# Optimization experiments

Hardware: AMD Instinct MI355X
Metric: run time of the kernel (lower is better)

## Reference

```python
import jax, jax.numpy as jnp
import numpy as np

N, E, F_IN, H, K = 100000, 1600000, 256, 128, 5


def setup_inputs() -> dict:
    key = jax.random.key(0)
    ks = jax.random.split(key, 24)

    def rn(k, shape, scale=0.05):
        return jax.random.normal(k, shape, dtype=jnp.float32) * scale

    inp = {
        "x": rn(ks[0], (N, F_IN), 1.0),
        "edge_index": jax.random.randint(ks[1], (2, E), 0, N, dtype=jnp.int64),
        "edge_attr": jax.random.uniform(ks[2], (N, K), dtype=jnp.float32),
        "pre_W": rn(ks[3], (F_IN, H)),
        "pre_b": jnp.zeros((H,), jnp.float32),
        "c1_Ws": rn(ks[4], (H, H)),
        "c1_Wn": rn(ks[5], (H, H)),
        "c1_b": jnp.zeros((H,), jnp.float32),
        "c2_Ws": rn(ks[6], (H, H)),
        "c2_Wn": rn(ks[7], (H, H)),
        "c2_b": jnp.zeros((H,), jnp.float32),
        "nodepost_W": rn(ks[8], (H, H)),
        "nodepost_b": jnp.zeros((H,), jnp.float32),
        "d_W0": rn(ks[9], (K, H)),
        "d_b0": jnp.zeros((H,), jnp.float32),
        "d_W1": rn(ks[10], (H, H)),
        "d_b1": jnp.zeros((H,), jnp.float32),
        "d_W2": rn(ks[11], (H, H)),
        "d_b2": jnp.zeros((H,), jnp.float32),
        "d_W3": rn(ks[12], (H, H)),
        "d_b3": jnp.zeros((H,), jnp.float32),
        "final_W": rn(ks[13], (2 * H, 1)),
        "final_b": jnp.zeros((1,), jnp.float32),
    }
    return inp


def _mean_agg(h, src, dst, n):
    # scatter-mean of source features onto destination nodes
    s = jax.ops.segment_sum(h[src], dst, num_segments=n)  # [N, H]
    deg = jax.ops.segment_sum(jnp.ones_like(dst, dtype=h.dtype), dst, num_segments=n)
    return s / jnp.maximum(deg, 1.0)[:, None]


def reference(x, edge_index, edge_attr, pre_W, pre_b,
              c1_Ws, c1_Wn, c1_b, c2_Ws, c2_Wn, c2_b,
              nodepost_W, nodepost_b,
              d_W0, d_b0, d_W1, d_b1, d_W2, d_b2, d_W3, d_b3,
              final_W, final_b):
    n = x.shape[0]
    src, dst = edge_index[0], edge_index[1]

    # --- feat path: NodeAttributeAggregator ---
    h = x @ pre_W + pre_b                                   # pre_process_mlp
    agg = _mean_agg(h, src, dst, n)
    h = jax.nn.relu(h @ c1_Ws + agg @ c1_Wn + c1_b)          # layer1 conv + act
    agg = _mean_agg(h, src, dst, n)
    h = jax.nn.relu(h @ c2_Ws + agg @ c2_Wn + c2_b)          # layer2 conv + act
    feat_out = h @ nodepost_W + nodepost_b                   # post_process_mlp

    # --- dist path: EdgeAttributeAggregator (MLP over edge attrs) ---
    e = edge_attr.reshape(-1, K)
    y = jax.nn.relu(e @ d_W0 + d_b0)
    y = jax.nn.relu(y @ d_W1 + d_b1)
    y = jax.nn.relu(y @ d_W2 + d_b2)
    dist_out = y @ d_W3 + d_b3

    # --- merge 'cat' + final MLP + squeeze + sigmoid ---
    z = jnp.concatenate([feat_out, dist_out], axis=1)        # [N, 2H]
    out = (z @ final_W + final_b).squeeze(1)                  # [N]
    return jax.nn.sigmoid(out)
```

## Files before the change

kernel.cpp:

```cpp
#include <hip/hip_runtime.h>

#define HF 128
#define CAP 64
#define PSHIFT 17
#define BUCKET_BLOCKS 2048

typedef __attribute__((ext_vector_type(8))) short s16x8;
typedef __attribute__((ext_vector_type(4))) float f32x4;
typedef __attribute__((ext_vector_type(2))) float f32x2;

__device__ __forceinline__ unsigned short f2bf(float f) {
    unsigned u = __float_as_uint(f);
    return (unsigned short)((u + 0x7fff + ((u >> 16) & 1)) >> 16);
}

#if __has_builtin(__builtin_amdgcn_cvt_pk_fp8_f32) && __has_builtin(__builtin_amdgcn_cvt_pk_f32_fp8)
#define FP8_HW 1
#else
#define FP8_HW 0
#endif

__device__ __forceinline__ unsigned char f2fp8(float f) {
#if FP8_HW
    int v = __builtin_amdgcn_cvt_pk_fp8_f32(f, f, 0, false);
    return (unsigned char)(v & 0xff);
#else
    unsigned u = __float_as_uint(f);
    unsigned s = (u >> 24) & 0x80;
    float a = fabsf(f);
    if (a > 448.f) a = 448.f;
    if (a < 0.015625f) {
        int q = (int)(a * 512.f + 0.5f);
        return (unsigned char)(s | q);
    }
    unsigned ub = __float_as_uint(a);
    ub += 0x0007ffff + ((ub >> 20) & 1);
    int e8 = (int)(ub >> 23) - 127 + 7;
    if (e8 >= 16) return (unsigned char)(s | 0x7e);
    return (unsigned char)(s | (e8 << 3) | ((ub >> 20) & 7));
#endif
}

__device__ __forceinline__ void fp8acc4(unsigned w, float* acc) {
#if FP8_HW
    f32x2 lo = __builtin_amdgcn_cvt_pk_f32_fp8(w, false);
    f32x2 hi = __builtin_amdgcn_cvt_pk_f32_fp8(w, true);
    acc[0] += lo.x; acc[1] += lo.y; acc[2] += hi.x; acc[3] += hi.y;
#else
    #pragma unroll
    for (int j = 0; j < 4; ++j) {
        unsigned b = (w >> (8 * j)) & 0xff;
        unsigned s = (b >> 7) & 1, e = (b >> 3) & 15, m = b & 7;
        float v = e ? __uint_as_float(((e + 120) << 23) | (m << 20))
                    : (float)m * 0.001953125f;
        acc[j] += s ? -v : v;
    }
#endif
}

__device__ __forceinline__ void repack_one(
    const float* __restrict__ W, short* __restrict__ Wp, int K, int t)
{
    int nkt = K >> 5;
    int lane = t & 63;
    int kt = (t >> 6) % nkt;
    int nt = (t >> 6) / nkt;
    int c = nt * 16 + (lane & 15);
    int kbase = kt * 32 + (lane >> 4) * 8;
    s16x8 v;
    #pragma unroll
    for (int j = 0; j < 8; ++j) v[j] = (short)f2bf(W[(long)(kbase + j) * HF + c]);
    *(s16x8*)(Wp + (long)t * 8) = v;
}

__global__ __launch_bounds__(256) void repack_all(
    const float* __restrict__ preW, const float* __restrict__ c1Ws,
    const float* __restrict__ c1Wn, const float* __restrict__ c2Ws,
    const float* __restrict__ c2Wn, const float* __restrict__ dW1,
    const float* __restrict__ dW2,
    short* preWp, short* c1Wsp, short* c1Wnp, short* c2Wsp, short* c2Wnp,
    short* dW1p, short* dW2p,
    const float* __restrict__ npW, const float* __restrict__ npb,
    const float* __restrict__ dW3, const float* __restrict__ db3,
    const float* __restrict__ fW,  const float* __restrict__ fb,
    float* __restrict__ uvc)
{
    int b = blockIdx.x;
    if (b == 64) {
        int i = threadIdx.x;
        if (i < HF) {
            float u = 0.f, v = 0.f;
            for (int j = 0; j < HF; ++j) {
                u += npW[i * HF + j] * fW[j];
                v += dW3[i * HF + j] * fW[HF + j];
            }
            uvc[i] = u;
            uvc[HF + i] = v;
            if (i == 0) {
                float c = fb[0];
                for (int j = 0; j < HF; ++j) c += npb[j] * fW[j] + db3[j] * fW[HF + j];
                uvc[2 * HF] = c;
            }
        }
        return;
    }
    if (b < 16) { repack_one(preW, preWp, 256, b * 256 + threadIdx.x); return; }
    int m = (b - 16) >> 3, t = ((b - 16) & 7) * 256 + threadIdx.x;
    const float* W; short* Wp;
    switch (m) {
        case 0: W = c1Ws; Wp = c1Wsp; break;
        case 1: W = c1Wn; Wp = c1Wnp; break;
        case 2: W = c2Ws; Wp = c2Wsp; break;
        case 3: W = c2Wn; Wp = c2Wnp; break;
        case 4: W = dW1;  Wp = dW1p;  break;
        default: W = dW2; Wp = dW2p;  break;
    }
    repack_one(W, Wp, HF, t);
}

__global__ __launch_bounds__(256) void bucketx_kernel(
    const int* __restrict__ eidx, long E,
    int* __restrict__ deg, int* __restrict__ bucket, int npass)
{
    const int xcd   = blockIdx.x & 7;
    const int chunk = blockIdx.x >> 3;
    const int nchunks = BUCKET_BLOCKS / 8;
    long per = (E + nchunks - 1) / nchunks;
    per = (per + 3) & ~3L;
    const long e0 = (long)chunk * per;
    const long e1 = (e0 + per < E) ? e0 + per : E;
    if (e0 >= E) return;
    for (int p = 0; p < npass; ++p) {
        for (long e = e0 + (long)threadIdx.x * 4; e + 4 <= e1; e += 1024) {
            int4 d4 = *(const int4*)(eidx + E + e);
            #pragma unroll
            for (int j = 0; j < 4; ++j) {
                int d = (&d4.x)[j];
                if ((d >> PSHIFT) != p || ((d >> 4) & 7) != xcd) continue;
                int s = eidx[e + j];
                int pos = atomicAdd(&deg[d], 1);
                if (pos < CAP) bucket[(long)d * CAP + pos] = s;
            }
        }
        for (long e = (e1 & ~3L) + threadIdx.x; e < e1; e += 256) {
            int d = eidx[E + e];
            if ((d >> PSHIFT) != p || ((d >> 4) & 7) != xcd) continue;
            int s = eidx[e];
            int pos = atomicAdd(&deg[d], 1);
            if (pos < CAP) bucket[(long)d * CAP + pos] = s;
        }
    }
}

__device__ __forceinline__ void agg_tile512(
    const unsigned char* __restrict__ hq, const int* __restrict__ deg,
    const int* __restrict__ bucket, int n, long row0B, int wv, int lane,
    unsigned* lds)
{
    const int g = lane >> 4;
    const int i = lane & 15;
    #pragma unroll
    for (int it = 0; it < 2; ++it) {
        const int rl = wv * 8 + it * 4 + g;
        const long node = row0B + rl;
        float acc[8];
        #pragma unroll
        for (int j = 0; j < 8; ++j) acc[j] = 0.f;
        int dg = 0, m = 0;
        const int* bl = bucket;
        if (node < n) {
            dg = deg[node];
            m = dg < CAP ? dg : CAP;
            bl = bucket + node * CAP;
        }
        int e = 0;
        for (; e + 8 <= m; e += 8) {
            int4 sa = *(const int4*)(bl + e);
            int4 sb = *(const int4*)(bl + e + 4);
            uint2 v0 = *(const uint2*)(hq + (long)sa.x * HF + i * 8);
            uint2 v1 = *(const uint2*)(hq + (long)sa.y * HF + i * 8);
            uint2 v2 = *(const uint2*)(hq + (long)sa.z * HF + i * 8);
            uint2 v3 = *(const uint2*)(hq + (long)sa.w * HF + i * 8);
            uint2 v4 = *(const uint2*)(hq + (long)sb.x * HF + i * 8);
            uint2 v5 = *(const uint2*)(hq + (long)sb.y * HF + i * 8);
            uint2 v6 = *(const uint2*)(hq + (long)sb.z * HF + i * 8);
            uint2 v7 = *(const uint2*)(hq + (long)sb.w * HF + i * 8);
            fp8acc4(v0.x, acc); fp8acc4(v0.y, acc + 4);
            fp8acc4(v1.x, acc); fp8acc4(v1.y, acc + 4);
            fp8acc4(v2.x, acc); fp8acc4(v2.y, acc + 4);
            fp8acc4(v3.x, acc); fp8acc4(v3.y, acc + 4);
            fp8acc4(v4.x, acc); fp8acc4(v4.y, acc + 4);
            fp8acc4(v5.x, acc); fp8acc4(v5.y, acc + 4);
            fp8acc4(v6.x, acc); fp8acc4(v6.y, acc + 4);
            fp8acc4(v7.x, acc); fp8acc4(v7.y, acc + 4);
        }
        for (; e + 4 <= m; e += 4) {
            int4 sa = *(const int4*)(bl + e);
            uint2 v0 = *(const uint2*)(hq + (long)sa.x * HF + i * 8);
            uint2 v1 = *(const uint2*)(hq + (long)sa.y * HF + i * 8);
            uint2 v2 = *(const uint2*)(hq + (long)sa.z * HF + i * 8);
            uint2 v3 = *(const uint2*)(hq + (long)sa.w * HF + i * 8);
            fp8acc4(v0.x, acc); fp8acc4(v0.y, acc + 4);
            fp8acc4(v1.x, acc); fp8acc4(v1.y, acc + 4);
            fp8acc4(v2.x, acc); fp8acc4(v2.y, acc + 4);
            fp8acc4(v3.x, acc); fp8acc4(v3.y, acc + 4);
        }
        for (; e < m; ++e) {
            uint2 v = *(const uint2*)(hq + (long)bl[e] * HF + i * 8);
            fp8acc4(v.x, acc); fp8acc4(v.y, acc + 4);
        }
        const float sc = 1.f / (float)(dg > 1 ? dg : 1);
        uint4 o;
        o.x = (unsigned)f2bf(acc[0] * sc) | ((unsigned)f2bf(acc[1] * sc) << 16);
        o.y = (unsigned)f2bf(acc[2] * sc) | ((unsigned)f2bf(acc[3] * sc) << 16);
        o.z = (unsigned)f2bf(acc[4] * sc) | ((unsigned)f2bf(acc[5] * sc) << 16);
        o.w = (unsigned)f2bf(acc[6] * sc) | ((unsigned)f2bf(acc[7] * sc) << 16);
        *(uint4*)&lds[rl * 64 + ((i ^ (rl & 15)) << 2)] = o;
    }
}

__device__ __forceinline__ void gemm_pass4(
    const unsigned short* __restrict__ Av, const short* __restrict__ Wp,
    long rA, int lane, int nb, f32x4 acc[4])
{
    const int q = lane >> 4;
    #pragma unroll
    for (int kt = 0; kt < 4; ++kt) {
        s16x8 a = *(const s16x8*)(Av + rA * HF + kt * 32 + q * 8);
        #pragma unroll
        for (int j = 0; j < 4; ++j) {
            s16x8 b = *(const s16x8*)(Wp + ((long)((nb + j) * 4 + kt) * 64 + lane) * 8);
            acc[j] = __builtin_amdgcn_mfma_f32_16x16x32_bf16(a, b, acc[j], 0, 0, 0);
        }
    }
}

__device__ __forceinline__ void gemm_pass_lds4(
    const unsigned* lds, int w3, int lane, const short* __restrict__ Wp,
    int nb, f32x4 acc[4])
{
    const int q = lane >> 4;
    const int i15 = lane & 15;
    const int rl = w3 * 16 + i15;
    #pragma unroll
    for (int kt = 0; kt < 4; ++kt) {
        s16x8 a = *(const s16x8*)&lds[rl * 64 + (((kt * 4 + q) ^ i15) << 2)];
        #pragma unroll
        for (int j = 0; j < 4; ++j) {
            s16x8 b = *(const s16x8*)(Wp + ((long)((nb + j) * 4 + kt) * 64 + lane) * 8);
            acc[j] = __builtin_amdgcn_mfma_f32_16x16x32_bf16(a, b, acc[j], 0, 0, 0);
        }
    }
}

__device__ __forceinline__ void gemm_pass_mfma8(
    const unsigned short* __restrict__ Av, const short* __restrict__ Wp,
    long rA, int lane, f32x4 acc[8])
{
    const int q = lane >> 4;
    #pragma unroll
    for (int kt = 0; kt < 4; ++kt) {
        s16x8 a = *(const s16x8*)(Av + rA * HF + kt * 32 + q * 8);
        #pragma unroll
        for (int nt = 0; nt < 8; ++nt) {
            s16x8 b = *(const s16x8*)(Wp + ((long)(nt * 4 + kt) * 64 + lane) * 8);
            acc[nt] = __builtin_amdgcn_mfma_f32_16x16x32_bf16(a, b, acc[nt], 0, 0, 0);
        }
    }
}

__device__ __forceinline__ void gemm_pass_lds8(
    const unsigned* lds, int w3, int lane, const short* __restrict__ Wp, f32x4 acc[8])
{
    const int q = lane >> 4;
    const int i15 = lane & 15;
    const int rl = w3 * 16 + i15;
    #pragma unroll
    for (int kt = 0; kt < 4; ++kt) {
        s16x8 a = *(const s16x8*)&lds[rl * 64 + (((kt * 4 + q) ^ i15) << 2)];
        #pragma unroll
        for (int nt = 0; nt < 8; ++nt) {
            s16x8 b = *(const s16x8*)(Wp + ((long)(nt * 4 + kt) * 64 + lane) * 8);
            acc[nt] = __builtin_amdgcn_mfma_f32_16x16x32_bf16(a, b, acc[nt], 0, 0, 0);
        }
    }
}

__global__ __launch_bounds__(512) void prek_kernel(
    const float* __restrict__ x, const short* __restrict__ preWp,
    const float* __restrict__ preb, unsigned short* __restrict__ h0,
    unsigned char* __restrict__ h0q, int n)
{
    __shared__ float ldsx[64 * 256];
    const int lane = threadIdx.x & 63;
    const int wv   = threadIdx.x >> 6;
    const long row0B = (long)blockIdx.x * 64;

    #pragma unroll
    for (int rr = 0; rr < 8; ++rr) {
        const int row = wv * 8 + rr;
        const long gr = row0B + row;
        if (gr < n) {
            const int s = row & 7;
            const float* gp = x + gr * 256 + ((lane ^ s) << 2);
#if __has_builtin(__builtin_amdgcn_global_load_lds)
            __builtin_amdgcn_global_load_lds(
                (const __attribute__((address_space(1))) void*)gp,
                (__attribute__((address_space(3))) void*)&ldsx[row * 256], 16, 0, 0);
#else
            float4 f = *(const float4*)gp;
            *(float4*)&ldsx[row * 256 + lane * 4] = f;
#endif
        }
    }
    __syncthreads();

    const int w3 = wv & 3;
    const int nb = (wv >> 2) * 4;
    const int q  = lane >> 4;
    const int l15 = lane & 15;
    const int rl = w3 * 16 + l15;
    const int s  = rl & 7;

    f32x4 acc[4];
    #pragma unroll
    for (int j = 0; j < 4; ++j)
        #pragma unroll
        for (int i = 0; i < 4; ++i) acc[j][i] = 0.f;

    #pragma unroll
    for (int kt = 0; kt < 8; ++kt) {
        const int c0 = kt * 8 + q * 2;
        float4 f0 = *(const float4*)&ldsx[rl * 256 + ((c0 ^ s) << 2)];
        float4 f1 = *(const float4*)&ldsx[rl * 256 + (((c0 + 1) ^ s) << 2)];
        s16x8 a;
        a[0] = (short)f2bf(f0.x); a[1] = (short)f2bf(f0.y);
        a[2] = (short)f2bf(f0.z); a[3] = (short)f2bf(f0.w);
        a[4] = (short)f2bf(f1.x); a[5] = (short)f2bf(f1.y);
        a[6] = (short)f2bf(f1.z); a[7] = (short)f2bf(f1.w);
        #pragma unroll
        for (int j = 0; j < 4; ++j) {
            s16x8 b = *(const s16x8*)(preWp + ((long)((nb + j) * 8 + kt) * 64 + lane) * 8);
            acc[j] = __builtin_amdgcn_mfma_f32_16x16x32_bf16(a, b, acc[j], 0, 0, 0);
        }
    }
    __syncthreads();

    unsigned short* lp16 = (unsigned short*)ldsx;
    unsigned char*  lp8  = (unsigned char*)ldsx + 16384;
    const int cq = lane >> 4;
    #pragma unroll
    for (int j = 0; j < 4; ++j) {
        int col = (nb + j) * 16 + l15;
        float bs = preb[col];
        #pragma unroll
        for (int i = 0; i < 4; ++i) {
            int row = w3 * 16 + cq * 4 + i;
            float o = acc[j][i] + bs;
            lp16[row * 128 + col] = f2bf(o);
            lp8[row * 128 + col]  = f2fp8(o);
        }
    }
    __syncthreads();

    const int r = threadIdx.x >> 3;
    const int c = (threadIdx.x & 7) * 16;
    const long gr = row0B + r;
    if (gr < n) {
        uint4* src = (uint4*)&lp16[r * 128 + c];
        *(uint4*)(h0 + gr * HF + c)     = src[0];
        *(uint4*)(h0 + gr * HF + c + 8) = src[1];
        *(uint4*)(h0q + gr * HF + c)    = *(uint4*)&lp8[r * 128 + c];
    }
}

__global__ __launch_bounds__(512) void disthead_kernel(
    const float* __restrict__ ea, const float* __restrict__ W0,
    const float* __restrict__ b0, const short* __restrict__ W1p,
    const float* __restrict__ b1, unsigned short* __restrict__ y1, int n)
{
    __shared__ unsigned short lpk[64 * 128];
    const int lane = threadIdx.x & 63;
    const int wv   = threadIdx.x >> 6;
    const int w3   = wv & 3;
    const int nb   = (wv >> 2) * 4;
    const long row0B = (long)blockIdx.x * 64;
    const long row0 = row0B + w3 * 16;
    const int q = lane >> 4;
    long rA = row0 + (lane & 15);
    if (rA > n - 1) rA = n - 1;

    float e0 = ea[rA * 5 + 0], e1 = ea[rA * 5 + 1], e2 = ea[rA * 5 + 2],
          e3 = ea[rA * 5 + 3], e4 = ea[rA * 5 + 4];

    f32x4 acc[4];
    #pragma unroll
    for (int j = 0; j < 4; ++j)
        #pragma unroll
        for (int i = 0; i < 4; ++i) acc[j][i] = 0.f;

    #pragma unroll
    for (int kt = 0; kt < 4; ++kt) {
        const int c = kt * 32 + q * 8;
        s16x8 a;
        #pragma unroll
        for (int h = 0; h < 2; ++h) {
            float4 w0 = *(const float4*)(W0 + 0 * HF + c + h * 4);
            float4 w1 = *(const float4*)(W0 + 1 * HF + c + h * 4);
            float4 w2 = *(const float4*)(W0 + 2 * HF + c + h * 4);
            float4 w3v = *(const float4*)(W0 + 3 * HF + c + h * 4);
            float4 w4 = *(const float4*)(W0 + 4 * HF + c + h * 4);
            float4 bb = *(const float4*)(b0 + c + h * 4);
            float z0 = fmaxf(bb.x + e0 * w0.x + e1 * w1.x + e2 * w2.x + e3 * w3v.x + e4 * w4.x, 0.f);
            float z1 = fmaxf(bb.y + e0 * w0.y + e1 * w1.y + e2 * w2.y + e3 * w3v.y + e4 * w4.y, 0.f);
            float z2 = fmaxf(bb.z + e0 * w0.z + e1 * w1.z + e2 * w2.z + e3 * w3v.z + e4 * w4.z, 0.f);
            float z3 = fmaxf(bb.w + e0 * w0.w + e1 * w1.w + e2 * w2.w + e3 * w3v.w + e4 * w4.w, 0.f);
            a[h * 4 + 0] = (short)f2bf(z0); a[h * 4 + 1] = (short)f2bf(z1);
            a[h * 4 + 2] = (short)f2bf(z2); a[h * 4 + 3] = (short)f2bf(z3);
        }
        #pragma unroll
        for (int j = 0; j < 4; ++j) {
            s16x8 b = *(const s16x8*)(W1p + ((long)((nb + j) * 4 + kt) * 64 + lane) * 8);
            acc[j] = __builtin_amdgcn_mfma_f32_16x16x32_bf16(a, b, acc[j], 0, 0, 0);
        }
    }

    const int cq = lane >> 4;
    const int l15 = lane & 15;
    #pragma unroll
    for (int j = 0; j < 4; ++j) {
        int col = (nb + j) * 16 + l15;
        float bs = b1[col];
        #pragma unroll
        for (int i = 0; i < 4; ++i) {
            int row = w3 * 16 + cq * 4 + i;
            lpk[row * 128 + col] = f2bf(fmaxf(acc[j][i] + bs, 0.f));
        }
    }
    __syncthreads();

    const int r = threadIdx.x >> 3;
    const int c = (threadIdx.x & 7) * 16;
    const long gr = row0B + r;
    if (gr < n) {
        uint4* src = (uint4*)&lpk[r * 128 + c];
        *(uint4*)(y1 + gr * HF + c)     = src[0];
        *(uint4*)(y1 + gr * HF + c + 8) = src[1];
    }
}

__global__ __launch_bounds__(512) void c1f_kernel(
    const unsigned short* __restrict__ h0, const unsigned char* __restrict__ h0q,
    const int* __restrict__ deg, const int* __restrict__ bucket,
    const short* __restrict__ Wsp, const short* __restrict__ Wnp,
    const float* __restrict__ bias, unsigned short* __restrict__ out,
    unsigned char* __restrict__ outq, int n)
{
    __shared__ unsigned ldsagg[64 * 64];
    const int lane = threadIdx.x & 63;
    const int wv   = threadIdx.x >> 6;
    const long row0B = (long)blockIdx.x * 64;

    agg_tile512(h0q, deg, bucket, n, row0B, wv, lane, ldsagg);
    __syncthreads();

    const int w3 = wv & 3;
    const int nb = (wv >> 2) * 4;

    f32x4 acc[4];
    #pragma unroll
    for (int j = 0; j < 4; ++j)
        #pragma unroll
        for (int i = 0; i < 4; ++i) acc[j][i] = 0.f;

    const long row0 = row0B + w3 * 16;
    long rA = row0 + (lane & 15);
    if (rA > n - 1) rA = n - 1;

    gemm_pass4(h0, Wsp, rA, lane, nb, acc);
    gemm_pass_lds4(ldsagg, w3, lane, Wnp, nb, acc);

    const int cq = lane >> 4;
    #pragma unroll
    for (int j = 0; j < 4; ++j) {
        int col = (nb + j) * 16 + (lane & 15);
        float bs = bias[col];
        #pragma unroll
        for (int i = 0; i < 4; ++i) {
            long r = row0 + cq * 4 + i;
            if (r < n) {
                float o = fmaxf(acc[j][i] + bs, 0.f);
                out[r * HF + col] = f2bf(o);
                outq[r * HF + col] = f2fp8(o);
            }
        }
    }
}

__global__ __launch_bounds__(512) void tailf_kernel(
    const unsigned short* __restrict__ h1, const unsigned char* __restrict__ h1q,
    const unsigned short* __restrict__ y1,
    const int* __restrict__ deg, const int* __restrict__ bucket,
    const short* __restrict__ c2Wsp, const short* __restrict__ c2Wnp,
    const short* __restrict__ dW2p,
    const float* __restrict__ c2b, const float* __restrict__ db2,
    const float* __restrict__ uvc, float* __restrict__ out, int n)
{
    __shared__ unsigned ldsagg[64 * 64];
    __shared__ float pp[2][64];
    const int lane = threadIdx.x & 63;
    const int wv   = threadIdx.x >> 6;
    const long row0B = (long)blockIdx.x * 64;

    agg_tile512(h1q, deg, bucket, n, row0B, wv, lane, ldsagg);
    __syncthreads();

    const int w = wv & 3;
    const long row0 = row0B + w * 16;
    long rA = row0 + (lane & 15);
    if (rA > n - 1) rA = n - 1;
    const int cq = lane >> 4;
    float part[4] = {0.f, 0.f, 0.f, 0.f};

    f32x4 acc[8];
    #pragma unroll
    for (int nt = 0; nt < 8; ++nt)
        #pragma unroll
        for (int i = 0; i < 4; ++i) acc[nt][i] = 0.f;

    if (wv < 4) {
        gemm_pass_mfma8(h1, c2Wsp, rA, lane, acc);
        gemm_pass_lds8(ldsagg, w, lane, c2Wnp, acc);
        #pragma unroll
        for (int nt = 0; nt < 8; ++nt) {
            int col = nt * 16 + (lane & 15);
            float bh = c2b[col], uu = uvc[col];
            #pragma unroll
            for (int i = 0; i < 4; ++i)
                part[i] += fmaxf(acc[nt][i] + bh, 0.f) * uu;
        }
    } else {
        gemm_pass_mfma8(y1, dW2p, rA, lane, acc);
        #pragma unroll
        for (int nt = 0; nt < 8; ++nt) {
            int col = nt * 16 + (lane & 15);
            float by = db2[col], vv = uvc[HF + col];
            #pragma unroll
            for (int i = 0; i < 4; ++i)
                part[i] += fmaxf(acc[nt][i] + by, 0.f) * vv;
        }
    }

    #pragma unroll
    for (int i = 0; i < 4; ++i) {
        float s = part[i];
        s += __shfl_xor(s, 1, 64);
        s += __shfl_xor(s, 2, 64);
        s += __shfl_xor(s, 4, 64);
        s += __shfl_xor(s, 8, 64);
        part[i] = s;
    }
    if ((lane & 15) == 0) {
        #pragma unroll
        for (int i = 0; i < 4; ++i)
            pp[wv >> 2][w * 16 + cq * 4 + i] = part[i];
    }
    __syncthreads();

    if (threadIdx.x < 64) {
        long r = row0B + threadIdx.x;
        if (r < n) {
            float s = pp[0][threadIdx.x] + pp[1][threadIdx.x] + uvc[2 * HF];
            out[r] = 1.f / (1.f + expf(-s));
        }
    }
}

extern "C" void kernel_launch(void* const* d_in, const int* in_sizes, int n_in,
                              void* d_out, int out_size, void* d_ws, size_t ws_size,
                              hipStream_t stream)
{
    const float* x      = (const float*)d_in[0];
    const int*   eidx   = (const int*)  d_in[1];
    const float* eattr  = (const float*)d_in[2];
    const float* pre_W  = (const float*)d_in[3];
    const float* pre_b  = (const float*)d_in[4];
    const float* c1_Ws  = (const float*)d_in[5];
    const float* c1_Wn  = (const float*)d_in[6];
    const float* c1_b   = (const float*)d_in[7];
    const float* c2_Ws  = (const float*)d_in[8];
    const float* c2_Wn  = (const float*)d_in[9];
    const float* c2_b   = (const float*)d_in[10];
    const float* npW    = (const float*)d_in[11];
    const float* npb    = (const float*)d_in[12];
    const float* dW0    = (const float*)d_in[13];
    const float* db0    = (const float*)d_in[14];
    const float* dW1    = (const float*)d_in[15];
    const float* db1    = (const float*)d_in[16];
    const float* dW2    = (const float*)d_in[17];
    const float* db2    = (const float*)d_in[18];
    const float* dW3    = (const float*)d_in[19];
    const float* db3    = (const float*)d_in[20];
    const float* fW     = (const float*)d_in[21];
    const float* fb     = (const float*)d_in[22];

    const int  n = in_sizes[0] / 256;
    const long E = in_sizes[1] / 2;

    char* ws = (char*)d_ws;
    size_t off = 0;
    auto alloc = [&](size_t bytes) -> void* {
        void* p = ws + off;
        off += (bytes + 255) & ~(size_t)255;
        return p;
    };
    unsigned short* B0 = (unsigned short*)alloc((size_t)n * HF * 2);
    unsigned short* B1 = (unsigned short*)alloc((size_t)n * HF * 2);
    unsigned short* B2 = (unsigned short*)alloc((size_t)n * HF * 2);
    unsigned char*  B0q = (unsigned char*)alloc((size_t)n * HF);
    unsigned char*  B1q = (unsigned char*)alloc((size_t)n * HF);
    int*   deg    = (int*)alloc((size_t)n * sizeof(int));
    int*   bucket = (int*)alloc((size_t)n * CAP * sizeof(int));
    float* uvc    = (float*)alloc((2 * HF + 1) * sizeof(float));
    short* preWp  = (short*)alloc(256 * HF * 2);
    short* c1Wsp  = (short*)alloc(HF * HF * 2);
    short* c1Wnp  = (short*)alloc(HF * HF * 2);
    short* c2Wsp  = (short*)alloc(HF * HF * 2);
    short* c2Wnp  = (short*)alloc(HF * HF * 2);
    short* dW1p   = (short*)alloc(HF * HF * 2);
    short* dW2p   = (short*)alloc(HF * HF * 2);

    const int gemmBlocks = (n + 63) / 64;
    const int npass = ((n - 1) >> PSHIFT) + 1;

    repack_all<<<65, 256, 0, stream>>>(
        pre_W, c1_Ws, c1_Wn, c2_Ws, c2_Wn, dW1, dW2,
        preWp, c1Wsp, c1Wnp, c2Wsp, c2Wnp, dW1p, dW2p,
        npW, npb, dW3, db3, fW, fb, uvc);

    hipMemsetAsync(deg, 0, (size_t)n * sizeof(int), stream);

    bucketx_kernel<<<BUCKET_BLOCKS, 256, 0, stream>>>(eidx, E, deg, bucket, npass);

    prek_kernel<<<gemmBlocks, 512, 0, stream>>>(x, preWp, pre_b, B0, B0q, n);

    disthead_kernel<<<gemmBlocks, 512, 0, stream>>>(
        eattr, dW0, db0, dW1p, db1, B2, n);

    c1f_kernel<<<gemmBlocks, 512, 0, stream>>>(
        B0, B0q, deg, bucket, c1Wsp, c1Wnp, c1_b, B1, B1q, n);

    tailf_kernel<<<gemmBlocks, 512, 0, stream>>>(
        B1, B1q, B2, deg, bucket, c2Wsp, c2Wnp, dW2p, c2_b, db2, uvc, (float*)d_out, n);
}
```

Before: 315.1 us.

## Stage neighbor buckets in LDS and gather 16-byte fp8 rows per lane

Each block now copies its 64 nodes' bucket lists and degrees into LDS with coalesced 16-byte loads before aggregating, instead of reading bucket indices from global memory inside the gather loop. The gather is restructured so 8 lanes cover one 128-byte fp8 row with 16-byte loads, giving 8 rows per wave in a single pass, and the loop runs to the wave's maximum degree with predicated accumulation. This aims for wider, fewer memory transactions and less index-load latency. The cost is extra LDS, a barrier, wasted lanes when degrees within a wave differ, and a full CAP-wide bucket copy even for low-degree nodes, so the bucket buffer is padded.

```diff
diff --git a/kernel.cpp b/kernel.cpp
--- a/kernel.cpp
+++ b/kernel.cpp
@@ -4,6 +4,7 @@
 #define CAP 64
 #define PSHIFT 17
 #define BUCKET_BLOCKS 2048
+#define BKS 68
 
 typedef __attribute__((ext_vector_type(8))) short s16x8;
 typedef __attribute__((ext_vector_type(4))) float f32x4;
@@ -152,71 +153,81 @@
     }
 }
 
-__device__ __forceinline__ void agg_tile512(
-    const unsigned char* __restrict__ hq, const int* __restrict__ deg,
-    const int* __restrict__ bucket, int n, long row0B, int wv, int lane,
-    unsigned* lds)
-{
-    const int g = lane >> 4;
-    const int i = lane & 15;
-    #pragma unroll
-    for (int it = 0; it < 2; ++it) {
-        const int rl = wv * 8 + it * 4 + g;
-        const long node = row0B + rl;
-        float acc[8];
-        #pragma unroll
-        for (int j = 0; j < 8; ++j) acc[j] = 0.f;
-        int dg = 0, m = 0;
-        const int* bl = bucket;
-        if (node < n) {
-            dg = deg[node];
-            m = dg < CAP ? dg : CAP;
-            bl = bucket + node * CAP;
-        }
-        int e = 0;
-        for (; e + 8 <= m; e += 8) {
-            int4 sa = *(const int4*)(bl + e);
-            int4 sb = *(const int4*)(bl + e + 4);
-            uint2 v0 = *(const uint2*)(hq + (long)sa.x * HF + i * 8);
-            uint2 v1 = *(const uint2*)(hq + (long)sa.y * HF + i * 8);
-            uint2 v2 = *(const uint2*)(hq + (long)sa.z * HF + i * 8);
-            uint2 v3 = *(const uint2*)(hq + (long)sa.w * HF + i * 8);
-            uint2 v4 = *(const uint2*)(hq + (long)sb.x * HF + i * 8);
-            uint2 v5 = *(const uint2*)(hq + (long)sb.y * HF + i * 8);
-            uint2 v6 = *(const uint2*)(hq + (long)sb.z * HF + i * 8);
-            uint2 v7 = *(const uint2*)(hq + (long)sb.w * HF + i * 8);
-            fp8acc4(v0.x, acc); fp8acc4(v0.y, acc + 4);
-            fp8acc4(v1.x, acc); fp8acc4(v1.y, acc + 4);
-            fp8acc4(v2.x, acc); fp8acc4(v2.y, acc + 4);
-            fp8acc4(v3.x, acc); fp8acc4(v3.y, acc + 4);
-            fp8acc4(v4.x, acc); fp8acc4(v4.y, acc + 4);
-            fp8acc4(v5.x, acc); fp8acc4(v5.y, acc + 4);
-            fp8acc4(v6.x, acc); fp8acc4(v6.y, acc + 4);
-            fp8acc4(v7.x, acc); fp8acc4(v7.y, acc + 4);
-        }
-        for (; e + 4 <= m; e += 4) {
-            int4 sa = *(const int4*)(bl + e);
-            uint2 v0 = *(const uint2*)(hq + (long)sa.x * HF + i * 8);
-            uint2 v1 = *(const uint2*)(hq + (long)sa.y * HF + i * 8);
-            uint2 v2 = *(const uint2*)(hq + (long)sa.z * HF + i * 8);
-            uint2 v3 = *(const uint2*)(hq + (long)sa.w * HF + i * 8);
-            fp8acc4(v0.x, acc); fp8acc4(v0.y, acc + 4);
-            fp8acc4(v1.x, acc); fp8acc4(v1.y, acc + 4);
-            fp8acc4(v2.x, acc); fp8acc4(v2.y, acc + 4);
-            fp8acc4(v3.x, acc); fp8acc4(v3.y, acc + 4);
-        }
-        for (; e < m; ++e) {
-            uint2 v = *(const uint2*)(hq + (long)bl[e] * HF + i * 8);
-            fp8acc4(v.x, acc); fp8acc4(v.y, acc + 4);
-        }
-        const float sc = 1.f / (float)(dg > 1 ? dg : 1);
-        uint4 o;
-        o.x = (unsigned)f2bf(acc[0] * sc) | ((unsigned)f2bf(acc[1] * sc) << 16);
-        o.y = (unsigned)f2bf(acc[2] * sc) | ((unsigned)f2bf(acc[3] * sc) << 16);
-        o.z = (unsigned)f2bf(acc[4] * sc) | ((unsigned)f2bf(acc[5] * sc) << 16);
-        o.w = (unsigned)f2bf(acc[6] * sc) | ((unsigned)f2bf(acc[7] * sc) << 16);
-        *(uint4*)&lds[rl * 64 + ((i ^ (rl & 15)) << 2)] = o;
-    }
+__device__ __forceinline__ void stage_bucket(
+    const int* __restrict__ bucket, const int* __restrict__ deg,
+    long row0B, int n, int* ldsbkt, int* ldsdeg)
+{
+    const uint4* gb = (const uint4*)(bucket + row0B * CAP);
+    #pragma unroll
+    for (int h = 0; h < 2; ++h) {
+        int u = threadIdx.x + h * 512;
+        int row = u >> 4, q = u & 15;
+        *(uint4*)&ldsbkt[row * BKS + q * 4] = gb[u];
+    }
+    if (threadIdx.x < 64) {
+        long node = row0B + threadIdx.x;
+        ldsdeg[threadIdx.x] = (node < n) ? deg[node] : 0;
+    }
+}
+
+__device__ __forceinline__ void agg_tile_v2(
+    const unsigned char* __restrict__ hq,
+    const int* ldsbkt, const int* ldsdeg,
+    int n, long row0B, int wv, int lane, unsigned* ldsagg)
+{
+    const int r = lane >> 3;
+    const int i = lane & 7;
+    const int rg = wv * 8 + r;
+
+    const int dg = ldsdeg[rg];
+    const int m  = dg < CAP ? dg : CAP;
+    int maxm = m;
+    maxm = max(maxm, __shfl_xor(maxm, 8, 64));
+    maxm = max(maxm, __shfl_xor(maxm, 16, 64));
+    maxm = max(maxm, __shfl_xor(maxm, 32, 64));
+
+    float acc[16];
+    #pragma unroll
+    for (int j = 0; j < 16; ++j) acc[j] = 0.f;
+
+    const int* bl = ldsbkt + rg * BKS;
+    for (int e = 0; e < maxm; e += 8) {
+        int4 ia = *(const int4*)(bl + e);
+        int4 ib = *(const int4*)(bl + e + 4);
+        int s0 = (e + 0 < m) ? ia.x : 0;
+        int s1 = (e + 1 < m) ? ia.y : 0;
+        int s2 = (e + 2 < m) ? ia.z : 0;
+        int s3 = (e + 3 < m) ? ia.w : 0;
+        int s4 = (e + 4 < m) ? ib.x : 0;
+        int s5 = (e + 5 < m) ? ib.y : 0;
+        int s6 = (e + 6 < m) ? ib.z : 0;
+        int s7 = (e + 7 < m) ? ib.w : 0;
+        uint4 v0 = *(const uint4*)(hq + (long)s0 * HF + i * 16);
+        uint4 v1 = *(const uint4*)(hq + (long)s1 * HF + i * 16);
+        uint4 v2 = *(const uint4*)(hq + (long)s2 * HF + i * 16);
+        uint4 v3 = *(const uint4*)(hq + (long)s3 * HF + i * 16);
+        uint4 v4 = *(const uint4*)(hq + (long)s4 * HF + i * 16);
+        uint4 v5 = *(const uint4*)(hq + (long)s5 * HF + i * 16);
+        uint4 v6 = *(const uint4*)(hq + (long)s6 * HF + i * 16);
+        uint4 v7 = *(const uint4*)(hq + (long)s7 * HF + i * 16);
+        if (e + 0 < m) { fp8acc4(v0.x, acc); fp8acc4(v0.y, acc + 4); fp8acc4(v0.z, acc + 8); fp8acc4(v0.w, acc + 12); }
+        if (e + 1 < m) { fp8acc4(v1.x, acc); fp8acc4(v1.y, acc + 4); fp8acc4(v1.z, acc + 8); fp8acc4(v1.w, acc + 12); }
+        if (e + 2 < m) { fp8acc4(v2.x, acc); fp8acc4(v2.y, acc + 4); fp8acc4(v2.z, acc + 8); fp8acc4(v2.w, acc + 12); }
+        if (e + 3 < m) { fp8acc4(v3.x, acc); fp8acc4(v3.y, acc + 4); fp8acc4(v3.z, acc + 8); fp8acc4(v3.w, acc + 12); }
+        if (e + 4 < m) { fp8acc4(v4.x, acc); fp8acc4(v4.y, acc + 4); fp8acc4(v4.z, acc + 8); fp8acc4(v4.w, acc + 12); }
+        if (e + 5 < m) { fp8acc4(v5.x, acc); fp8acc4(v5.y, acc + 4); fp8acc4(v5.z, acc + 8); fp8acc4(v5.w, acc + 12); }
+        if (e + 6 < m) { fp8acc4(v6.x, acc); fp8acc4(v6.y, acc + 4); fp8acc4(v6.z, acc + 8); fp8acc4(v6.w, acc + 12); }
+        if (e + 7 < m) { fp8acc4(v7.x, acc); fp8acc4(v7.y, acc + 4); fp8acc4(v7.z, acc + 8); fp8acc4(v7.w, acc + 12); }
+    }
+
+    const float sc = 1.f / (float)(dg > 1 ? dg : 1);
+    unsigned pk[8];
+    #pragma unroll
+    for (int j = 0; j < 8; ++j)
+        pk[j] = (unsigned)f2bf(acc[2 * j] * sc) | ((unsigned)f2bf(acc[2 * j + 1] * sc) << 16);
+    const int c0 = 2 * i, c1 = 2 * i + 1, s = rg & 15;
+    *(uint4*)&ldsagg[rg * 64 + ((c0 ^ s) << 2)] = make_uint4(pk[0], pk[1], pk[2], pk[3]);
+    *(uint4*)&ldsagg[rg * 64 + ((c1 ^ s) << 2)] = make_uint4(pk[4], pk[5], pk[6], pk[7]);
 }
 
 __device__ __forceinline__ void gemm_pass4(
@@ -457,11 +468,15 @@
     unsigned char* __restrict__ outq, int n)
 {
     __shared__ unsigned ldsagg[64 * 64];
+    __shared__ int ldsbkt[64 * BKS];
+    __shared__ int ldsdeg[64];
     const int lane = threadIdx.x & 63;
     const int wv   = threadIdx.x >> 6;
     const long row0B = (long)blockIdx.x * 64;
 
-    agg_tile512(h0q, deg, bucket, n, row0B, wv, lane, ldsagg);
+    stage_bucket(bucket, deg, row0B, n, ldsbkt, ldsdeg);
+    __syncthreads();
+    agg_tile_v2(h0q, ldsbkt, ldsdeg, n, row0B, wv, lane, ldsagg);
     __syncthreads();
 
     const int w3 = wv & 3;
@@ -507,12 +522,16 @@
     const float* __restrict__ uvc, float* __restrict__ out, int n)
 {
     __shared__ unsigned ldsagg[64 * 64];
+    __shared__ int ldsbkt[64 * BKS];
+    __shared__ int ldsdeg[64];
     __shared__ float pp[2][64];
     const int lane = threadIdx.x & 63;
     const int wv   = threadIdx.x >> 6;
     const long row0B = (long)blockIdx.x * 64;
 
-    agg_tile512(h1q, deg, bucket, n, row0B, wv, lane, ldsagg);
+    stage_bucket(bucket, deg, row0B, n, ldsbkt, ldsdeg);
+    __syncthreads();
+    agg_tile_v2(h1q, ldsbkt, ldsdeg, n, row0B, wv, lane, ldsagg);
     __syncthreads();
 
     const int w = wv & 3;
@@ -620,7 +639,7 @@
     unsigned char*  B0q = (unsigned char*)alloc((size_t)n * HF);
     unsigned char*  B1q = (unsigned char*)alloc((size_t)n * HF);
     int*   deg    = (int*)alloc((size_t)n * sizeof(int));
-    int*   bucket = (int*)alloc((size_t)n * CAP * sizeof(int));
+    int*   bucket = (int*)alloc(((size_t)n + 64) * CAP * sizeof(int));
     float* uvc    = (float*)alloc((2 * HF + 1) * sizeof(float));
     short* preWp  = (short*)alloc(256 * HF * 2);
     short* c1Wsp  = (short*)alloc(HF * HF * 2);
```

New measurement: 283.5 us. -10.0%, faster.
